# Kernel optimization log

Measured on AMD Instinct MI355X. Metric: run time of the kernel, lower is better.

Reference implementation:

```python
import jax, jax.numpy as jnp
import numpy as np

N_QUBITS = 11
DIM = 2 ** N_QUBITS
N_LAYERS = 6  # the circuit repeats the RY/CZ block 6 times


def _apply_ry(state, wire, theta):
    """Apply RY(theta) on `wire`. state: [N] + [2]*N_QUBITS (real, since RY/CZ are real).
    theta is scalar (shared weight) or [N] (per-sample input angle)."""
    half = theta * 0.5
    c, s = jnp.cos(half), jnp.sin(half)
    if c.ndim == 1:  # per-sample angle -> broadcast over remaining qubit axes
        bshape = (c.shape[0],) + (1,) * (N_QUBITS - 1)
        c = c.reshape(bshape)
        s = s.reshape(bshape)
    st = jnp.moveaxis(state, wire + 1, -1)  # [..., 2]
    s0, s1 = st[..., 0], st[..., 1]
    # RY = [[cos, -sin], [sin, cos]] acting on the qubit amplitude pair
    st = jnp.stack([c * s0 - s * s1, s * s0 + c * s1], axis=-1)
    return jnp.moveaxis(st, -1, wire + 1)


def _apply_cz(state, w1, w2):
    """CZ: flip sign of amplitudes where both qubits are |1>."""
    def bit(w):
        shp = [1] * (N_QUBITS + 1)
        shp[w + 1] = 2
        return jnp.array([0.0, 1.0], state.dtype).reshape(shp)
    sign = 1.0 - 2.0 * bit(w1) * bit(w2)
    return state * sign


def _circuit(angles, weights):
    # angles: [N, N_QUBITS] per-sample RY input angles; weights: [N_QUBITS]
    N = angles.shape[0]
    state = jnp.zeros((N, DIM), angles.dtype).at[:, 0].set(1.0)  # |0...0>
    state = state.reshape((N,) + (2,) * N_QUBITS)
    for i in range(N_QUBITS):
        state = _apply_ry(state, i, angles[:, i])
    for _ in range(N_LAYERS):
        for i in range(N_QUBITS):
            state = _apply_ry(state, i, weights[i])
            state = _apply_cz(state, i, (i + 1) % N_QUBITS)
    probs = state.reshape(N, DIM) ** 2  # real state -> |amp|^2
    # PauliZ expectation per wire; wire 0 is the most-significant bit (PennyLane order)
    bits = (jnp.arange(DIM)[:, None] >> jnp.arange(N_QUBITS - 1, -1, -1)[None, :]) & 1
    z = (1.0 - 2.0 * bits).astype(angles.dtype)  # [DIM, N_QUBITS]
    return probs @ z  # [N, N_QUBITS]


def setup_inputs() -> dict:
    key = jax.random.key(0)
    kx, kw = jax.random.split(key)
    x = jax.random.normal(kx, (8, 256, 16), dtype=jnp.float32)
    weights = jax.random.normal(kw, (N_QUBITS,), dtype=jnp.float32)
    return {"x": x, "weights": weights}


def reference(x, weights):
    B, T, _ = x.shape
    # every (b, t) sample is an independent circuit -> batch them all together
    angles = x[:, :, :N_QUBITS].reshape(B * T, N_QUBITS)
    out = _circuit(angles, weights)  # [B*T, N_QUBITS]
    return out.reshape(B, T, N_QUBITS)
```

## Files before the change

### kernel.cpp

```cpp
#include <hip/hip_runtime.h>

#define NQ 11


typedef float f32x2 __attribute__((ext_vector_type(2)));

__device__ __forceinline__ f32x2 b2(float s) { f32x2 r; r.x = s; r.y = s; return r; }
__device__ __forceinline__ f32x2 fma2(f32x2 a, f32x2 b, f32x2 c) {
    return __builtin_elementwise_fma(a, b, c);
}

template <int CTRL>
__device__ __forceinline__ float dpp_mov(float x) {
    const int xi = __builtin_bit_cast(int, x);
    return __builtin_bit_cast(float,
        __builtin_amdgcn_update_dpp(xi, xi, CTRL, 0xf, 0xf, false));
}
#define DPP_XOR1 0xB1
#define DPP_XOR2 0x4E
#define DPP_XOR3 0x1B
#define DPP_XOR7 0x141
#define DPP_XOR8 0x128

#define RY_K_F(KB, KSB, C, S)                                                \
    _Pragma("unroll")                                                        \
    for (int g = 0; g < 8; ++g) {                                            \
        const int k0 = ((g >> (KB)) << ((KB) + 1)) | (g & ((1 << (KB)) - 1));\
        const int k1 = k0 | (1 << (KB));                                     \
        const f32x2 a_ = v2[k0], b_ = v2[k1];                                \
        const f32x2 Cv = b2(C), Sv = b2(S);                                  \
        if (k0 & (KSB)) {                                                    \
            v2[k0] = fma2(Cv, a_, Sv * b_);                                  \
            v2[k1] = fma2(Sv, a_, -(Cv * b_));                               \
        } else {                                                             \
            v2[k0] = fma2(Cv, a_, -(Sv * b_));                               \
            v2[k1] = fma2(Sv, a_, Cv * b_);                                  \
        }                                                                    \
    }

#define RY_DS_B(SHFL, CV, SV)                                                \
    {                                                                        \
        f32x2 pa_[16];                                                       \
        _Pragma("unroll")                                                    \
        for (int k = 0; k < 16; ++k) {                                       \
            pa_[k].x = SHFL(v2[k].x);                                        \
            pa_[k].y = SHFL(v2[k].y);                                        \
        }                                                                    \
        _Pragma("unroll")                                                    \
        for (int k = 0; k < 16; ++k)                                         \
            v2[k] = fma2(CV, v2[k], (SV) * pa_[k]);                          \
    }

#define RY_DPP(PGETX, CV, SV)                                                \
    _Pragma("unroll")                                                        \
    for (int k = 0; k < 16; ++k) {                                           \
        f32x2 pa_;                                                           \
        pa_.x = PGETX(v2[k].x);                                              \
        pa_.y = PGETX(v2[k].y);                                              \
        v2[k] = fma2(CV, v2[k], (SV) * pa_);                                 \
    }

__global__ __launch_bounds__(256, 2) void qru_kernel(
    const float* __restrict__ x,
    const float* __restrict__ w,
    float* __restrict__ out)
{
    const int lane = threadIdx.x & 63;
    const int n    = blockIdx.x * 4 + (threadIdx.x >> 6);

    const float4 xa = *(const float4*)(x + n * 16);
    const float4 xb = *(const float4*)(x + n * 16 + 4);
    const float4 xc = *(const float4*)(x + n * 16 + 8);
    const float xv[NQ] = {xa.x, xa.y, xa.z, xa.w, xb.x, xb.y, xb.z, xb.w,
                          xc.x, xc.y, xc.z};
    float ci[NQ], si[NQ];
#pragma unroll
    for (int q = 0; q < NQ; ++q) {
        const float h = xv[q] * 0.5f;
        si[q] = __sinf(h); ci[q] = __cosf(h);
    }
    float cw[NQ], sw[NQ];
#pragma unroll
    for (int q = 0; q < NQ; ++q) {
        const float h = w[q] * 0.5f;
        sw[q] = __sinf(h); cw[q] = __cosf(h);
    }

    const float laneF =
        ((lane & 32) ? si[5]  : ci[5])  *
        ((lane & 16) ? si[6]  : ci[6])  *
        ((lane & 8)  ? si[7]  : ci[7])  *
        ((lane & 4)  ? si[8]  : ci[8])  *
        ((lane & 2)  ? si[9]  : ci[9])  *
        ((lane & 1)  ? si[10] : ci[10]);

    f32x2 v2[16];
#pragma unroll
    for (int k = 0; k < 16; ++k) {
        const float base = laneF * ((k & 8) ? si[0] : ci[0])
                                 * ((k & 4) ? si[1] : ci[1])
                                 * ((k & 2) ? si[2] : ci[2])
                                 * ((k & 1) ? si[3] : ci[3]);
        v2[k].x = base * ci[4];
        v2[k].y = base * si[4];
    }

    const float X0m = (lane & 1) ?  sw[0] : -sw[0];
    const float Y0m = (lane & 1) ? -cw[0] :  cw[0];
    const float SS5 = (lane & 32) ?  sw[5] : -sw[5];
    const float C5m = (lane & 32) ? -cw[5] :  cw[5];
    f32x2 Cv5; Cv5.x = cw[5]; Cv5.y = C5m;
    f32x2 Sv5; Sv5.x = SS5;   Sv5.y = sw[5];
    const f32x2 C6v  = b2(((lane & 48) == 48) ? -cw[6]  : cw[6]);
    const f32x2 S6v  = b2((lane & 48) ? sw[6]  : -sw[6]);
    const f32x2 C7v  = b2(((lane & 24) == 24) ? -cw[7]  : cw[7]);
    const f32x2 S7v  = b2((lane & 24) ? sw[7]  : -sw[7]);
    const f32x2 C8v  = b2(((lane & 12) == 12) ? -cw[8]  : cw[8]);
    const f32x2 S8v  = b2((lane & 12) ? sw[8]  : -sw[8]);
    const f32x2 C9v  = b2(((lane & 6)  == 6)  ? -cw[9]  : cw[9]);
    const f32x2 S9v  = b2((lane & 6)  ? sw[9]  : -sw[9]);
    const f32x2 C10v = b2(((lane & 3)  == 3)  ? -cw[10] : cw[10]);
    const f32x2 S10v = b2((lane & 3)  ? sw[10] : -sw[10]);

    f32x2 C4p; C4p.x = cw[4];  C4p.y =  cw[4];
    f32x2 S4p; S4p.x = -sw[4]; S4p.y =  sw[4];
    f32x2 C4m; C4m.x = cw[4];  C4m.y = -cw[4];
    f32x2 S4m; S4m.x = sw[4];  S4m.y =  sw[4];

    auto shfl32 = [](float t) { return __shfl_xor(t, 32); };
    auto shfl16 = [](float t) { return __shfl_xor(t, 16); };
    auto dppx8  = [](float t) { return dpp_mov<DPP_XOR8>(t); };
    auto dppx4  = [](float t) { return dpp_mov<DPP_XOR3>(dpp_mov<DPP_XOR7>(t)); };
    auto dppx2  = [](float t) { return dpp_mov<DPP_XOR2>(t); };
    auto dppx1  = [](float t) { return dpp_mov<DPP_XOR1>(t); };

    auto layer = [&](float X0, float Y0) {
        {
            const f32x2 c0 = b2(cw[0]), s0 = b2(sw[0]);
            const f32x2 x0 = b2(X0),    y0 = b2(Y0);
#pragma unroll
            for (int k = 0; k < 8; ++k) {
                const f32x2 a_ = v2[k], b_ = v2[k | 8];
                v2[k]     = fma2(c0, a_, x0 * b_);
                v2[k | 8] = fma2(s0, a_, y0 * b_);
            }
        }
        RY_K_F(2, 8, cw[1], sw[1])
        RY_K_F(1, 4, cw[2], sw[2])
        RY_K_F(0, 2, cw[3], sw[3])

#pragma unroll
        for (int k = 0; k < 16; ++k) {
            const f32x2 s_ = __builtin_shufflevector(v2[k], v2[k], 1, 0);
            v2[k] = (k & 1) ? fma2(C4m, v2[k], S4m * s_)
                            : fma2(C4p, v2[k], S4p * s_);
        }

        RY_DS_B(shfl32, Cv5, Sv5)
        RY_DS_B(shfl16, C6v, S6v)
        RY_DPP(dppx8,  C7v,  S7v)
        RY_DPP(dppx4,  C8v,  S8v)
        RY_DPP(dppx2,  C9v,  S9v)
        RY_DPP(dppx1,  C10v, S10v)
    };

    layer(-sw[0], cw[0]);
#pragma unroll 1
    for (int l = 1; l < 6; ++l) layer(X0m, Y0m);

    f32x2 T = b2(0.f), A3 = b2(0.f), A2 = b2(0.f), A1 = b2(0.f), A0 = b2(0.f);
#pragma unroll
    for (int k = 0; k < 16; ++k) {
        const f32x2 p = v2[k] * v2[k];
        T = T + p;
        if (k & 8) A3 = A3 + p;
        if (k & 4) A2 = A2 + p;
        if (k & 2) A1 = A1 + p;
        if (k & 1) A0 = A0 + p;
    }
    const float tot = T.x + T.y;

    float q[NQ];
    q[0] = tot - 2.f * (A3.x + A3.y);
    q[1] = tot - 2.f * (A2.x + A2.y);
    q[2] = tot - 2.f * (A1.x + A1.y);
    q[3] = tot - 2.f * (A0.x + A0.y);
    q[4] = tot - 2.f * T.y;
    q[5]  = (lane & 32) ? -tot : tot;
    q[6]  = (lane & 16) ? -tot : tot;
    q[7]  = (lane & 8)  ? -tot : tot;
    q[8]  = (lane & 4)  ? -tot : tot;
    q[9]  = (lane & 2)  ? -tot : tot;
    q[10] = (lane & 1)  ? -tot : tot;

#pragma unroll
    for (int wq = 0; wq < NQ; ++wq) q[wq] += __shfl_xor(q[wq], 32);
#pragma unroll
    for (int wq = 0; wq < NQ; ++wq) q[wq] += __shfl_xor(q[wq], 16);
#pragma unroll
    for (int wq = 0; wq < NQ; ++wq) q[wq] += dpp_mov<DPP_XOR8>(q[wq]);
#pragma unroll
    for (int wq = 0; wq < NQ; ++wq)
        q[wq] += dpp_mov<DPP_XOR3>(dpp_mov<DPP_XOR7>(q[wq]));
#pragma unroll
    for (int wq = 0; wq < NQ; ++wq) q[wq] += dpp_mov<DPP_XOR2>(q[wq]);
#pragma unroll
    for (int wq = 0; wq < NQ; ++wq) q[wq] += dpp_mov<DPP_XOR1>(q[wq]);

    if (lane == 0) {
#pragma unroll
        for (int wq = 0; wq < NQ; ++wq) out[n * 11 + wq] = q[wq];
    }
}

extern "C" void kernel_launch(void* const* d_in, const int* in_sizes, int n_in,
                              void* d_out, int out_size, void* d_ws, size_t ws_size,
                              hipStream_t stream) {
    const float* x = (const float*)d_in[0];
    const float* w = (const float*)d_in[1];
    float* out = (float*)d_out;

    qru_kernel<<<512, 256, 0, stream>>>(x, w, out);
}
```

Measured before the change: 24.85 us.

## Split each circuit's state across two wavefronts exchanging qubit-0 via LDS

Each sample's 2048-amplitude state is now split between two wavefronts, with the qubit-0 half selected by wave index, so each thread holds 8 instead of 16 float pairs. The qubit-0 rotation becomes an exchange through double-buffered shared memory with a block barrier every layer. Partial expectation values are combined through shared memory at the end. The grid doubles and the occupancy hint rises, trading lower register pressure and more parallelism for per-layer LDS traffic and __syncthreads cost.

```diff
diff --git a/kernel.cpp b/kernel.cpp
--- a/kernel.cpp
+++ b/kernel.cpp
@@ -22,51 +22,58 @@
 #define DPP_XOR7 0x141
 #define DPP_XOR8 0x128
 
-#define RY_K_F(KB, KSB, C, S)                                                \
+#define RY_K_F8(KB, KSB, C, S)                                               \
     _Pragma("unroll")                                                        \
-    for (int g = 0; g < 8; ++g) {                                            \
+    for (int g = 0; g < 4; ++g) {                                            \
         const int k0 = ((g >> (KB)) << ((KB) + 1)) | (g & ((1 << (KB)) - 1));\
         const int k1 = k0 | (1 << (KB));                                     \
-        const f32x2 a_ = v2[k0], b_ = v2[k1];                                \
+        const f32x2 a_ = v2[k0], bb_ = v2[k1];                               \
         const f32x2 Cv = b2(C), Sv = b2(S);                                  \
         if (k0 & (KSB)) {                                                    \
-            v2[k0] = fma2(Cv, a_, Sv * b_);                                  \
-            v2[k1] = fma2(Sv, a_, -(Cv * b_));                               \
+            v2[k0] = fma2(Cv, a_, Sv * bb_);                                 \
+            v2[k1] = fma2(Sv, a_, -(Cv * bb_));                              \
         } else {                                                             \
-            v2[k0] = fma2(Cv, a_, -(Sv * b_));                               \
-            v2[k1] = fma2(Sv, a_, Cv * b_);                                  \
+            v2[k0] = fma2(Cv, a_, -(Sv * bb_));                              \
+            v2[k1] = fma2(Sv, a_, Cv * bb_);                                 \
         }                                                                    \
     }
 
-#define RY_DS_B(SHFL, CV, SV)                                                \
+#define RY_DS_B8(SHFL, CV, SV)                                               \
     {                                                                        \
-        f32x2 pa_[16];                                                       \
+        f32x2 pa_[8];                                                        \
         _Pragma("unroll")                                                    \
-        for (int k = 0; k < 16; ++k) {                                       \
+        for (int k = 0; k < 8; ++k) {                                        \
             pa_[k].x = SHFL(v2[k].x);                                        \
             pa_[k].y = SHFL(v2[k].y);                                        \
         }                                                                    \
         _Pragma("unroll")                                                    \
-        for (int k = 0; k < 16; ++k)                                         \
+        for (int k = 0; k < 8; ++k)                                          \
             v2[k] = fma2(CV, v2[k], (SV) * pa_[k]);                          \
     }
 
-#define RY_DPP(PGETX, CV, SV)                                                \
+#define RY_DPP8(PGETX, CV, SV)                                               \
     _Pragma("unroll")                                                        \
-    for (int k = 0; k < 16; ++k) {                                           \
+    for (int k = 0; k < 8; ++k) {                                            \
         f32x2 pa_;                                                           \
         pa_.x = PGETX(v2[k].x);                                              \
         pa_.y = PGETX(v2[k].y);                                              \
         v2[k] = fma2(CV, v2[k], (SV) * pa_);                                 \
     }
 
-__global__ __launch_bounds__(256, 2) void qru_kernel(
+__global__ __launch_bounds__(256, 4) void qru_kernel(
     const float* __restrict__ x,
     const float* __restrict__ w,
     float* __restrict__ out)
 {
-    const int lane = threadIdx.x & 63;
-    const int n    = blockIdx.x * 4 + (threadIdx.x >> 6);
+    const int tid  = threadIdx.x;
+    const int lane = tid & 63;
+    const int wid  = tid >> 6;
+    const int sloc = wid >> 1;
+    const int b    = wid & 1;
+    const int n    = blockIdx.x * 2 + sloc;
+
+    __shared__ f32x2 buf[2][4][8][64];
+    __shared__ float qbuf[4][12];
 
     const float4 xa = *(const float4*)(x + n * 16);
     const float4 xb = *(const float4*)(x + n * 16 + 4);
@@ -93,22 +100,32 @@
         ((lane & 4)  ? si[8]  : ci[8])  *
         ((lane & 2)  ? si[9]  : ci[9])  *
         ((lane & 1)  ? si[10] : ci[10]);
-
-    f32x2 v2[16];
-#pragma unroll
-    for (int k = 0; k < 16; ++k) {
-        const float base = laneF * ((k & 8) ? si[0] : ci[0])
-                                 * ((k & 4) ? si[1] : ci[1])
-                                 * ((k & 2) ? si[2] : ci[2])
-                                 * ((k & 1) ? si[3] : ci[3]);
+    const float B0 = (b ? si[0] : ci[0]) * laneF;
+
+    f32x2 v2[8];
+#pragma unroll
+    for (int k = 0; k < 8; ++k) {
+        const float base = B0 * ((k & 4) ? si[1] : ci[1])
+                              * ((k & 2) ? si[2] : ci[2])
+                              * ((k & 1) ? si[3] : ci[3]);
         v2[k].x = base * ci[4];
         v2[k].y = base * si[4];
     }
 
-    const float X0m = (lane & 1) ?  sw[0] : -sw[0];
-    const float Y0m = (lane & 1) ? -cw[0] :  cw[0];
-    const float SS5 = (lane & 32) ?  sw[5] : -sw[5];
-    const float C5m = (lane & 32) ? -cw[5] :  cw[5];
+    const int l0 = lane & 1;
+    const float CC0 = cw[0];
+    const float PP0 = b ? sw[0] : -sw[0];
+    const float CCm = b ? (l0 ? -cw[0] : cw[0]) : cw[0];
+    const float PPm = b ? sw[0] : (l0 ? sw[0] : -sw[0]);
+    const float S1n = b ? sw[1] : -sw[1];
+    const float C1n = b ? -cw[1] : cw[1];
+    f32x2 C4p; C4p.x = cw[4];  C4p.y =  cw[4];
+    f32x2 S4p; S4p.x = -sw[4]; S4p.y =  sw[4];
+    f32x2 C4m; C4m.x = cw[4];  C4m.y = -cw[4];
+    f32x2 S4m; S4m.x = sw[4];  S4m.y =  sw[4];
+    const bool hi5 = (lane & 32) != 0;
+    const float SS5 = hi5 ?  sw[5] : -sw[5];
+    const float C5m = hi5 ? -cw[5] :  cw[5];
     f32x2 Cv5; Cv5.x = cw[5]; Cv5.y = C5m;
     f32x2 Sv5; Sv5.x = SS5;   Sv5.y = sw[5];
     const f32x2 C6v  = b2(((lane & 48) == 48) ? -cw[6]  : cw[6]);
@@ -122,11 +139,6 @@
     const f32x2 C10v = b2(((lane & 3)  == 3)  ? -cw[10] : cw[10]);
     const f32x2 S10v = b2((lane & 3)  ? sw[10] : -sw[10]);
 
-    f32x2 C4p; C4p.x = cw[4];  C4p.y =  cw[4];
-    f32x2 S4p; S4p.x = -sw[4]; S4p.y =  sw[4];
-    f32x2 C4m; C4m.x = cw[4];  C4m.y = -cw[4];
-    f32x2 S4m; S4m.x = sw[4];  S4m.y =  sw[4];
-
     auto shfl32 = [](float t) { return __shfl_xor(t, 32); };
     auto shfl16 = [](float t) { return __shfl_xor(t, 16); };
     auto dppx8  = [](float t) { return dpp_mov<DPP_XOR8>(t); };
@@ -134,46 +146,54 @@
     auto dppx2  = [](float t) { return dpp_mov<DPP_XOR2>(t); };
     auto dppx1  = [](float t) { return dpp_mov<DPP_XOR1>(t); };
 
-    auto layer = [&](float X0, float Y0) {
+    auto layer = [&](int l, float CC, float PP) {
+#pragma unroll
+        for (int k = 0; k < 8; ++k) buf[l & 1][wid][k][lane] = v2[k];
+        __syncthreads();
+        f32x2 pr[8];
+#pragma unroll
+        for (int k = 0; k < 8; ++k) pr[k] = buf[l & 1][wid ^ 1][k][lane];
+        const f32x2 ccv = b2(CC), ppv = b2(PP);
+#pragma unroll
+        for (int k = 0; k < 8; ++k) v2[k] = fma2(ccv, v2[k], ppv * pr[k]);
+
         {
-            const f32x2 c0 = b2(cw[0]), s0 = b2(sw[0]);
-            const f32x2 x0 = b2(X0),    y0 = b2(Y0);
-#pragma unroll
-            for (int k = 0; k < 8; ++k) {
-                const f32x2 a_ = v2[k], b_ = v2[k | 8];
-                v2[k]     = fma2(c0, a_, x0 * b_);
-                v2[k | 8] = fma2(s0, a_, y0 * b_);
+            const f32x2 c1 = b2(cw[1]), s1 = b2(sw[1]);
+            const f32x2 s1n = b2(S1n), c1n = b2(C1n);
+#pragma unroll
+            for (int g = 0; g < 4; ++g) {
+                const f32x2 a_ = v2[g], bb_ = v2[g | 4];
+                v2[g]     = fma2(c1, a_, s1n * bb_);
+                v2[g | 4] = fma2(s1, a_, c1n * bb_);
             }
         }
-        RY_K_F(2, 8, cw[1], sw[1])
-        RY_K_F(1, 4, cw[2], sw[2])
-        RY_K_F(0, 2, cw[3], sw[3])
-
-#pragma unroll
-        for (int k = 0; k < 16; ++k) {
+        RY_K_F8(1, 4, cw[2], sw[2])
+        RY_K_F8(0, 2, cw[3], sw[3])
+
+#pragma unroll
+        for (int k = 0; k < 8; ++k) {
             const f32x2 s_ = __builtin_shufflevector(v2[k], v2[k], 1, 0);
             v2[k] = (k & 1) ? fma2(C4m, v2[k], S4m * s_)
                             : fma2(C4p, v2[k], S4p * s_);
         }
 
-        RY_DS_B(shfl32, Cv5, Sv5)
-        RY_DS_B(shfl16, C6v, S6v)
-        RY_DPP(dppx8,  C7v,  S7v)
-        RY_DPP(dppx4,  C8v,  S8v)
-        RY_DPP(dppx2,  C9v,  S9v)
-        RY_DPP(dppx1,  C10v, S10v)
+        RY_DS_B8(shfl32, Cv5, Sv5)
+        RY_DS_B8(shfl16, C6v, S6v)
+        RY_DPP8(dppx8,  C7v,  S7v)
+        RY_DPP8(dppx4,  C8v,  S8v)
+        RY_DPP8(dppx2,  C9v,  S9v)
+        RY_DPP8(dppx1,  C10v, S10v)
     };
 
-    layer(-sw[0], cw[0]);
+    layer(0, CC0, PP0);
 #pragma unroll 1
-    for (int l = 1; l < 6; ++l) layer(X0m, Y0m);
-
-    f32x2 T = b2(0.f), A3 = b2(0.f), A2 = b2(0.f), A1 = b2(0.f), A0 = b2(0.f);
-#pragma unroll
-    for (int k = 0; k < 16; ++k) {
+    for (int l = 1; l < 6; ++l) layer(l, CCm, PPm);
+
+    f32x2 T = b2(0.f), A2 = b2(0.f), A1 = b2(0.f), A0 = b2(0.f);
+#pragma unroll
+    for (int k = 0; k < 8; ++k) {
         const f32x2 p = v2[k] * v2[k];
         T = T + p;
-        if (k & 8) A3 = A3 + p;
         if (k & 4) A2 = A2 + p;
         if (k & 2) A1 = A1 + p;
         if (k & 1) A0 = A0 + p;
@@ -181,7 +201,7 @@
     const float tot = T.x + T.y;
 
     float q[NQ];
-    q[0] = tot - 2.f * (A3.x + A3.y);
+    q[0] = b ? -tot : tot;
     q[1] = tot - 2.f * (A2.x + A2.y);
     q[2] = tot - 2.f * (A1.x + A1.y);
     q[3] = tot - 2.f * (A0.x + A0.y);
@@ -209,7 +229,11 @@
 
     if (lane == 0) {
 #pragma unroll
-        for (int wq = 0; wq < NQ; ++wq) out[n * 11 + wq] = q[wq];
+        for (int wq = 0; wq < NQ; ++wq) qbuf[wid][wq] = q[wq];
+    }
+    __syncthreads();
+    if (b == 0 && lane < NQ) {
+        out[n * NQ + lane] = qbuf[wid][lane] + qbuf[wid + 1][lane];
     }
 }
 
@@ -220,5 +244,5 @@
     const float* w = (const float*)d_in[1];
     float* out = (float*)d_out;
 
-    qru_kernel<<<512, 256, 0, stream>>>(x, w, out);
-}
+    qru_kernel<<<1024, 256, 0, stream>>>(x, w, out);
+}
```

Result: slower. 27.65 us (+11.3%).
